# Kernel optimization log

Measured on AMD Instinct MI355X. Metric: run time of the kernel, lower is better.

Reference implementation:

```python
import jax, jax.numpy as jnp
import numpy as np

B = 16384
IN_DIM = 4096
H1, H2 = 128, 64
LATENT = 32
REPS = 3


def setup_inputs() -> dict:
    key = jax.random.key(0)
    ks = jax.random.split(key, 10)
    def lin(k, fan_in, fan_out):
        bound = 1.0 / np.sqrt(fan_in)
        kw, kb = jax.random.split(k)
        W = jax.random.uniform(kw, (fan_in, fan_out), jnp.float32, -bound, bound)
        b = jax.random.uniform(kb, (fan_out,), jnp.float32, -bound, bound)
        return W, b
    x = jax.random.normal(ks[0], (B, IN_DIM), jnp.float32)
    W1, b1 = lin(ks[1], IN_DIM, H1)
    W2, b2 = lin(ks[2], H1, H2)
    W3, b3 = lin(ks[3], H2, LATENT)
    qparams = jax.random.normal(ks[4], (REPS * 2 * LATENT,), jnp.float32)
    Wd, bd = lin(ks[5], LATENT, IN_DIM)
    return {"x": x, "W1": W1, "b1": b1, "W2": W2, "b2": b2,
            "W3": W3, "b3": b3, "qparams": qparams, "Wd": Wd, "bd": bd}


def _forward(x, W1, b1, W2, b2, W3, b3, qparams, Wd, bd):
    # Classical encoder (dropout inactive in eval mode)
    h = jax.nn.relu(x @ W1 + b1)          # [B, H1]
    h = jax.nn.relu(h @ W2 + b2)          # [B, H2]
    z = h @ W3 + b3                       # [B, LATENT]
    # Quantum decoder: circuit is AngleEmbedding (RX) of latent followed by
    # 2*REPS AngleEmbedding (RX) layers of params -- all RX on the same wire
    # commute and add, no entanglers => <Z_i> = cos(total angle on wire i).
    param_offset = qparams.reshape(2 * REPS, LATENT).sum(axis=0)  # [LATENT]
    q = jnp.cos(z + param_offset)         # [B, LATENT]
    # Classical decoder
    return q @ Wd + bd                    # [B, IN_DIM]


def reference(x, W1, b1, W2, b2, W3, b3, qparams, Wd, bd):
    return _forward(x, W1, b1, W2, b2, W3, b3, qparams, Wd, bd)
```

## Files before the change

### kernel.cpp

```cpp
#include <hip/hip_runtime.h>
#include <hip/hip_bf16.h>

#define B_SZ   16384
#define IN_DIM 4096
#define H1D    128
#define H2D    64
#define LAT    32

typedef _Float16 half8 __attribute__((ext_vector_type(8)));
typedef _Float16 half4 __attribute__((ext_vector_type(4)));
typedef float float4v __attribute__((ext_vector_type(4)));

#define WS_W2T  1048576
#define WS_W3T  1064960
#define WS_WDT  1069056
#define WS_B3O  1331200
#define WS_Q    1331328

__global__ __launch_bounds__(256) void prep_kernel(
    const float* __restrict__ W1, const float* __restrict__ W2,
    const float* __restrict__ W3, const float* __restrict__ Wd,
    const float* __restrict__ b3, const float* __restrict__ qp,
    _Float16* __restrict__ W1t, _Float16* __restrict__ W2t,
    _Float16* __restrict__ W3t, _Float16* __restrict__ Wdt,
    float* __restrict__ b3off)
{
    int t = blockIdx.x * 256 + threadIdx.x;
    if (t < IN_DIM * H1D) {
        int k = t >> 7, n = t & 127;
        W1t[n * IN_DIM + k] = (_Float16)W1[t];
    }
    if (t < LAT * IN_DIM) {
        int k = t >> 12, n = t & 4095;
        Wdt[n * LAT + k] = (_Float16)Wd[t];
    }
    if (t < H1D * H2D) {
        int k = t >> 6, n = t & 63;
        W2t[n * H1D + k] = (_Float16)W2[t];
    }
    if (t < H2D * LAT) {
        int k = t >> 5, n = t & 31;
        W3t[n * H2D + k] = (_Float16)W3[t];
    }
    if (t < LAT) {
        float s = b3[t];
        #pragma unroll
        for (int r = 0; r < 6; ++r) s += qp[r * LAT + t];
        b3off[t] = s;
    }
}

__global__ __launch_bounds__(512) void encoder_kernel(
    const float* __restrict__ x,
    const _Float16* __restrict__ W1t, const _Float16* __restrict__ W2t,
    const _Float16* __restrict__ W3t,
    const float* __restrict__ b1, const float* __restrict__ b2,
    const float* __restrict__ b3off, _Float16* __restrict__ qout)
{
    __shared__ alignas(16) char smem[27648];
    _Float16* xt  = (_Float16*)smem;
    _Float16* wt  = (_Float16*)(smem + 9216);
    _Float16* h1s = (_Float16*)smem;
    _Float16* h2s = (_Float16*)(smem + 17408);

    const int tid  = threadIdx.x;
    const int lane = tid & 63;
    const int w    = tid >> 6;
    const int l15  = lane & 15;
    const int quad = lane >> 4;
    const int rb0  = blockIdx.x * 64;

    const int wr = w >> 1;
    const int wc = w & 1;

    float4v acc[4];
    #pragma unroll
    for (int nt = 0; nt < 4; ++nt) {
        float bv = b1[wc * 64 + nt * 16 + l15];
        acc[nt] = (float4v){bv, bv, bv, bv};
    }

    for (int kit = 0; kit < IN_DIM / 64; ++kit) {
        #pragma unroll
        for (int i = 0; i < 2; ++i) {
            int idx = tid + i * 512;
            int r   = idx >> 4;
            int c4  = idx & 15;
            float4v xv = ((const float4v*)(x + (size_t)(rb0 + r) * IN_DIM + kit * 64))[c4];
            half4 p;
            p[0] = (_Float16)xv[0]; p[1] = (_Float16)xv[1];
            p[2] = (_Float16)xv[2]; p[3] = (_Float16)xv[3];
            *(half4*)(xt + r * 72 + c4 * 4) = p;
        }
        #pragma unroll
        for (int i = 0; i < 2; ++i) {
            int idx = tid + i * 512;
            int n   = idx >> 3;
            int c   = idx & 7;
            uint4 v = ((const uint4*)(W1t + (size_t)n * IN_DIM + kit * 64))[c];
            *(uint4*)(wt + n * 72 + c * 8) = v;
        }
        __syncthreads();
        #pragma unroll
        for (int ks = 0; ks < 2; ++ks) {
            half8 a = *(const half8*)(xt + (wr * 16 + l15) * 72 + ks * 32 + quad * 8);
            #pragma unroll
            for (int nt = 0; nt < 4; ++nt) {
                half8 b = *(const half8*)(wt + (wc * 64 + nt * 16 + l15) * 72 + ks * 32 + quad * 8);
                acc[nt] = __builtin_amdgcn_mfma_f32_16x16x32_f16(a, b, acc[nt], 0, 0, 0);
            }
        }
        __syncthreads();
    }

    #pragma unroll
    for (int nt = 0; nt < 4; ++nt) {
        int c = wc * 64 + nt * 16 + l15;
        #pragma unroll
        for (int r = 0; r < 4; ++r) {
            int row = wr * 16 + quad * 4 + r;
            float v = acc[nt][r];
            h1s[row * 136 + c] = (_Float16)(v > 0.f ? v : 0.f);
        }
    }
    __syncthreads();

    const int rb2 = (w & 3) * 16;
    const int wc2 = w >> 2;
    float4v acc2[2];
    #pragma unroll
    for (int nt = 0; nt < 2; ++nt) {
        float bv = b2[wc2 * 32 + nt * 16 + l15];
        acc2[nt] = (float4v){bv, bv, bv, bv};
    }
    #pragma unroll
    for (int ks = 0; ks < 4; ++ks) {
        half8 a = *(const half8*)(h1s + (rb2 + l15) * 136 + ks * 32 + quad * 8);
        #pragma unroll
        for (int nt = 0; nt < 2; ++nt) {
            int n = wc2 * 32 + nt * 16 + l15;
            half8 b = *(const half8*)(W2t + n * H1D + ks * 32 + quad * 8);
            acc2[nt] = __builtin_amdgcn_mfma_f32_16x16x32_f16(a, b, acc2[nt], 0, 0, 0);
        }
    }
    #pragma unroll
    for (int nt = 0; nt < 2; ++nt) {
        int c = wc2 * 32 + nt * 16 + l15;
        #pragma unroll
        for (int r = 0; r < 4; ++r) {
            int row = rb2 + quad * 4 + r;
            float v = acc2[nt][r];
            h2s[row * 72 + c] = (_Float16)(v > 0.f ? v : 0.f);
        }
    }
    __syncthreads();

    const int rb3 = (w & 3) * 16;
    const int wc3 = w >> 2;
    int c3 = wc3 * 16 + l15;
    float bv3 = b3off[c3];
    float4v acc3 = (float4v){bv3, bv3, bv3, bv3};
    #pragma unroll
    for (int ks = 0; ks < 2; ++ks) {
        half8 a = *(const half8*)(h2s + (rb3 + l15) * 72 + ks * 32 + quad * 8);
        half8 b = *(const half8*)(W3t + c3 * H2D + ks * 32 + quad * 8);
        acc3 = __builtin_amdgcn_mfma_f32_16x16x32_f16(a, b, acc3, 0, 0, 0);
    }
    #pragma unroll
    for (int r = 0; r < 4; ++r) {
        int row = rb0 + rb3 + quad * 4 + r;
        qout[(size_t)row * LAT + c3] = (_Float16)cosf(acc3[r]);
    }
}

__global__ __launch_bounds__(256) void decoder_kernel(
    const _Float16* __restrict__ qin, const _Float16* __restrict__ Wdt,
    const float* __restrict__ bd, float* __restrict__ out)
{
    __shared__ alignas(16) _Float16 qs[64 * 40];
    const int tid  = threadIdx.x;
    const int lane = tid & 63;
    const int w    = tid >> 6;
    const int l15  = lane & 15;
    const int quad = lane >> 4;
    const int rowBlk = blockIdx.x & 255;
    const int colBlk = blockIdx.x >> 8;
    const int rb = rowBlk * 64;
    const int cb = colBlk * 256 + w * 64;

    {
        int r = tid >> 2;
        int c = tid & 3;
        uint4 v = *((const uint4*)(qin + (size_t)(rb + r) * LAT) + c);
        *(uint4*)(qs + r * 40 + c * 8) = v;
    }
    __syncthreads();

    half8 a[4];
    #pragma unroll
    for (int mt = 0; mt < 4; ++mt)
        a[mt] = *(const half8*)(qs + (mt * 16 + l15) * 40 + quad * 8);

    #pragma unroll
    for (int nt = 0; nt < 4; ++nt) {
        int c = cb + nt * 16 + l15;
        half8 b = *(const half8*)(Wdt + (size_t)c * LAT + quad * 8);
        float bv = bd[c];
        float4v bias = (float4v){bv, bv, bv, bv};
        #pragma unroll
        for (int mt = 0; mt < 4; ++mt) {
            float4v o = __builtin_amdgcn_mfma_f32_16x16x32_f16(a[mt], b, bias, 0, 0, 0);
            #pragma unroll
            for (int r = 0; r < 4; ++r) {
                out[(size_t)(rb + mt * 16 + quad * 4 + r) * IN_DIM + c] = o[r];
            }
        }
    }
}

extern "C" void kernel_launch(void* const* d_in, const int* in_sizes, int n_in,
                              void* d_out, int out_size, void* d_ws, size_t ws_size,
                              hipStream_t stream)
{
    const float* x  = (const float*)d_in[0];
    const float* W1 = (const float*)d_in[1];
    const float* b1 = (const float*)d_in[2];
    const float* W2 = (const float*)d_in[3];
    const float* b2 = (const float*)d_in[4];
    const float* W3 = (const float*)d_in[5];
    const float* b3 = (const float*)d_in[6];
    const float* qp = (const float*)d_in[7];
    const float* Wd = (const float*)d_in[8];
    const float* bd = (const float*)d_in[9];
    float* out = (float*)d_out;

    char* ws = (char*)d_ws;
    _Float16* W1t = (_Float16*)(ws);
    _Float16* W2t = (_Float16*)(ws + WS_W2T);
    _Float16* W3t = (_Float16*)(ws + WS_W3T);
    _Float16* Wdt = (_Float16*)(ws + WS_WDT);
    float*    b3o = (float*)(ws + WS_B3O);
    _Float16* qbuf= (_Float16*)(ws + WS_Q);

    prep_kernel<<<2048, 256, 0, stream>>>(W1, W2, W3, Wd, b3, qp, W1t, W2t, W3t, Wdt, b3o);
    encoder_kernel<<<256, 512, 0, stream>>>(x, W1t, W2t, W3t, b1, b2, b3o, qbuf);
    decoder_kernel<<<4096, 256, 0, stream>>>(qbuf, Wdt, bd, out);
}
```

Baseline: 585.5 us.

## Use split-K register-direct encoder and LDS-staged coalesced decoder stores

The encoder now uses 32-row blocks with 256 threads, and each wave handles a quarter of the K dimension. Each wave loads x and W1t straight from global memory into MFMA operands without LDS staging or per-iteration barriers. The four partial sums are then reduced through shared memory before the small layers run. The decoder stages each 64x256 output tile in LDS and writes it back as row-contiguous float4 stores, and its block order is changed so consecutive blocks share rows. This trades extra LDS use and lower occupancy for fewer barriers, better parallelism with 512 blocks, and fully coalesced output writes.

```diff
diff --git a/kernel.cpp b/kernel.cpp
--- a/kernel.cpp
+++ b/kernel.cpp
@@ -50,143 +50,153 @@
     }
 }
 
-__global__ __launch_bounds__(512) void encoder_kernel(
+static __device__ __forceinline__ half8 cvt8(float4v v0, float4v v1) {
+    half8 h;
+    h[0] = (_Float16)v0[0]; h[1] = (_Float16)v0[1];
+    h[2] = (_Float16)v0[2]; h[3] = (_Float16)v0[3];
+    h[4] = (_Float16)v1[0]; h[5] = (_Float16)v1[1];
+    h[6] = (_Float16)v1[2]; h[7] = (_Float16)v1[3];
+    return h;
+}
+
+__global__ __launch_bounds__(256, 2) void encoder_kernel(
     const float* __restrict__ x,
     const _Float16* __restrict__ W1t, const _Float16* __restrict__ W2t,
     const _Float16* __restrict__ W3t,
     const float* __restrict__ b1, const float* __restrict__ b2,
     const float* __restrict__ b3off, _Float16* __restrict__ qout)
 {
-    __shared__ alignas(16) char smem[27648];
-    _Float16* xt  = (_Float16*)smem;
-    _Float16* wt  = (_Float16*)(smem + 9216);
-    _Float16* h1s = (_Float16*)smem;
-    _Float16* h2s = (_Float16*)(smem + 17408);
+    __shared__ alignas(16) float part[4 * 32 * 132];
+    __shared__ alignas(16) _Float16 h1s[32 * 136];
+    _Float16* h2s = (_Float16*)part;
 
     const int tid  = threadIdx.x;
     const int lane = tid & 63;
     const int w    = tid >> 6;
     const int l15  = lane & 15;
     const int quad = lane >> 4;
-    const int rb0  = blockIdx.x * 64;
-
-    const int wr = w >> 1;
-    const int wc = w & 1;
-
-    float4v acc[4];
-    #pragma unroll
-    for (int nt = 0; nt < 4; ++nt) {
-        float bv = b1[wc * 64 + nt * 16 + l15];
-        acc[nt] = (float4v){bv, bv, bv, bv};
-    }
-
-    for (int kit = 0; kit < IN_DIM / 64; ++kit) {
-        #pragma unroll
-        for (int i = 0; i < 2; ++i) {
-            int idx = tid + i * 512;
-            int r   = idx >> 4;
-            int c4  = idx & 15;
-            float4v xv = ((const float4v*)(x + (size_t)(rb0 + r) * IN_DIM + kit * 64))[c4];
-            half4 p;
-            p[0] = (_Float16)xv[0]; p[1] = (_Float16)xv[1];
-            p[2] = (_Float16)xv[2]; p[3] = (_Float16)xv[3];
-            *(half4*)(xt + r * 72 + c4 * 4) = p;
-        }
-        #pragma unroll
-        for (int i = 0; i < 2; ++i) {
-            int idx = tid + i * 512;
-            int n   = idx >> 3;
-            int c   = idx & 7;
-            uint4 v = ((const uint4*)(W1t + (size_t)n * IN_DIM + kit * 64))[c];
-            *(uint4*)(wt + n * 72 + c * 8) = v;
+    const int rb0  = blockIdx.x * 32;
+
+    float4v acc[2][8];
+    #pragma unroll
+    for (int mg = 0; mg < 2; ++mg)
+        #pragma unroll
+        for (int ct = 0; ct < 8; ++ct)
+            acc[mg][ct] = (float4v){0.f, 0.f, 0.f, 0.f};
+
+    const float* xp0 = x + (size_t)(rb0 + l15) * IN_DIM + w * 1024 + quad * 8;
+    const float* xp1 = xp0 + 16 * IN_DIM;
+    const _Float16* wp[8];
+    #pragma unroll
+    for (int ct = 0; ct < 8; ++ct)
+        wp[ct] = W1t + (size_t)(ct * 16 + l15) * IN_DIM + w * 1024 + quad * 8;
+
+    #pragma unroll 2
+    for (int kk = 0; kk < 32; ++kk) {
+        const int ko = kk * 32;
+        float4v x00 = *(const float4v*)(xp0 + ko);
+        float4v x01 = *(const float4v*)(xp0 + ko + 4);
+        float4v x10 = *(const float4v*)(xp1 + ko);
+        float4v x11 = *(const float4v*)(xp1 + ko + 4);
+        half8 a0 = cvt8(x00, x01);
+        half8 a1 = cvt8(x10, x11);
+        #pragma unroll
+        for (int ct = 0; ct < 8; ++ct) {
+            half8 b = *(const half8*)(wp[ct] + ko);
+            acc[0][ct] = __builtin_amdgcn_mfma_f32_16x16x32_f16(a0, b, acc[0][ct], 0, 0, 0);
+            acc[1][ct] = __builtin_amdgcn_mfma_f32_16x16x32_f16(a1, b, acc[1][ct], 0, 0, 0);
+        }
+    }
+
+    {
+        float* pw = part + w * (32 * 132);
+        #pragma unroll
+        for (int mg = 0; mg < 2; ++mg)
+            #pragma unroll
+            for (int ct = 0; ct < 8; ++ct)
+                #pragma unroll
+                for (int r = 0; r < 4; ++r)
+                    pw[(mg * 16 + quad * 4 + r) * 132 + ct * 16 + l15] = acc[mg][ct][r];
+    }
+    __syncthreads();
+
+    #pragma unroll
+    for (int i = 0; i < 4; ++i) {
+        int chunk = tid * 4 + i;
+        int row = chunk >> 5;
+        int c4  = chunk & 31;
+        const float* p = part + row * 132 + c4 * 4;
+        float4v s = *(const float4v*)(p)
+                  + *(const float4v*)(p + 32 * 132)
+                  + *(const float4v*)(p + 2 * 32 * 132)
+                  + *(const float4v*)(p + 3 * 32 * 132);
+        float4v bb = *(const float4v*)(b1 + c4 * 4);
+        s = s + bb;
+        half4 h;
+        h[0] = (_Float16)(s[0] > 0.f ? s[0] : 0.f);
+        h[1] = (_Float16)(s[1] > 0.f ? s[1] : 0.f);
+        h[2] = (_Float16)(s[2] > 0.f ? s[2] : 0.f);
+        h[3] = (_Float16)(s[3] > 0.f ? s[3] : 0.f);
+        *(half4*)(h1s + row * 136 + c4 * 4) = h;
+    }
+    __syncthreads();
+
+    {
+        float bv2 = b2[w * 16 + l15];
+        float4v a2[2] = {(float4v){bv2, bv2, bv2, bv2}, (float4v){bv2, bv2, bv2, bv2}};
+        #pragma unroll
+        for (int kk = 0; kk < 4; ++kk) {
+            half8 b = *(const half8*)(W2t + (w * 16 + l15) * H1D + kk * 32 + quad * 8);
+            half8 a0 = *(const half8*)(h1s + l15 * 136 + kk * 32 + quad * 8);
+            half8 a1 = *(const half8*)(h1s + (16 + l15) * 136 + kk * 32 + quad * 8);
+            a2[0] = __builtin_amdgcn_mfma_f32_16x16x32_f16(a0, b, a2[0], 0, 0, 0);
+            a2[1] = __builtin_amdgcn_mfma_f32_16x16x32_f16(a1, b, a2[1], 0, 0, 0);
         }
         __syncthreads();
         #pragma unroll
-        for (int ks = 0; ks < 2; ++ks) {
-            half8 a = *(const half8*)(xt + (wr * 16 + l15) * 72 + ks * 32 + quad * 8);
+        for (int mg = 0; mg < 2; ++mg)
             #pragma unroll
-            for (int nt = 0; nt < 4; ++nt) {
-                half8 b = *(const half8*)(wt + (wc * 64 + nt * 16 + l15) * 72 + ks * 32 + quad * 8);
-                acc[nt] = __builtin_amdgcn_mfma_f32_16x16x32_f16(a, b, acc[nt], 0, 0, 0);
+            for (int r = 0; r < 4; ++r) {
+                float v = a2[mg][r];
+                h2s[(mg * 16 + quad * 4 + r) * 72 + w * 16 + l15] = (_Float16)(v > 0.f ? v : 0.f);
             }
-        }
-        __syncthreads();
-    }
-
-    #pragma unroll
-    for (int nt = 0; nt < 4; ++nt) {
-        int c = wc * 64 + nt * 16 + l15;
+    }
+    __syncthreads();
+
+    {
+        const int mg3 = w >> 1;
+        const int ct3 = w & 1;
+        const int c3  = ct3 * 16 + l15;
+        float bv3 = b3off[c3];
+        float4v a3 = (float4v){bv3, bv3, bv3, bv3};
+        #pragma unroll
+        for (int kk = 0; kk < 2; ++kk) {
+            half8 a = *(const half8*)(h2s + (mg3 * 16 + l15) * 72 + kk * 32 + quad * 8);
+            half8 b = *(const half8*)(W3t + c3 * H2D + kk * 32 + quad * 8);
+            a3 = __builtin_amdgcn_mfma_f32_16x16x32_f16(a, b, a3, 0, 0, 0);
+        }
         #pragma unroll
         for (int r = 0; r < 4; ++r) {
-            int row = wr * 16 + quad * 4 + r;
-            float v = acc[nt][r];
-            h1s[row * 136 + c] = (_Float16)(v > 0.f ? v : 0.f);
-        }
-    }
-    __syncthreads();
-
-    const int rb2 = (w & 3) * 16;
-    const int wc2 = w >> 2;
-    float4v acc2[2];
-    #pragma unroll
-    for (int nt = 0; nt < 2; ++nt) {
-        float bv = b2[wc2 * 32 + nt * 16 + l15];
-        acc2[nt] = (float4v){bv, bv, bv, bv};
-    }
-    #pragma unroll
-    for (int ks = 0; ks < 4; ++ks) {
-        half8 a = *(const half8*)(h1s + (rb2 + l15) * 136 + ks * 32 + quad * 8);
-        #pragma unroll
-        for (int nt = 0; nt < 2; ++nt) {
-            int n = wc2 * 32 + nt * 16 + l15;
-            half8 b = *(const half8*)(W2t + n * H1D + ks * 32 + quad * 8);
-            acc2[nt] = __builtin_amdgcn_mfma_f32_16x16x32_f16(a, b, acc2[nt], 0, 0, 0);
-        }
-    }
-    #pragma unroll
-    for (int nt = 0; nt < 2; ++nt) {
-        int c = wc2 * 32 + nt * 16 + l15;
-        #pragma unroll
-        for (int r = 0; r < 4; ++r) {
-            int row = rb2 + quad * 4 + r;
-            float v = acc2[nt][r];
-            h2s[row * 72 + c] = (_Float16)(v > 0.f ? v : 0.f);
-        }
-    }
-    __syncthreads();
-
-    const int rb3 = (w & 3) * 16;
-    const int wc3 = w >> 2;
-    int c3 = wc3 * 16 + l15;
-    float bv3 = b3off[c3];
-    float4v acc3 = (float4v){bv3, bv3, bv3, bv3};
-    #pragma unroll
-    for (int ks = 0; ks < 2; ++ks) {
-        half8 a = *(const half8*)(h2s + (rb3 + l15) * 72 + ks * 32 + quad * 8);
-        half8 b = *(const half8*)(W3t + c3 * H2D + ks * 32 + quad * 8);
-        acc3 = __builtin_amdgcn_mfma_f32_16x16x32_f16(a, b, acc3, 0, 0, 0);
-    }
-    #pragma unroll
-    for (int r = 0; r < 4; ++r) {
-        int row = rb0 + rb3 + quad * 4 + r;
-        qout[(size_t)row * LAT + c3] = (_Float16)cosf(acc3[r]);
-    }
-}
-
-__global__ __launch_bounds__(256) void decoder_kernel(
+            int row = rb0 + mg3 * 16 + quad * 4 + r;
+            qout[(size_t)row * LAT + c3] = (_Float16)cosf(a3[r]);
+        }
+    }
+}
+
+__global__ __launch_bounds__(256, 2) void decoder_kernel(
     const _Float16* __restrict__ qin, const _Float16* __restrict__ Wdt,
     const float* __restrict__ bd, float* __restrict__ out)
 {
     __shared__ alignas(16) _Float16 qs[64 * 40];
+    __shared__ alignas(16) float ot[64 * 260];
     const int tid  = threadIdx.x;
     const int lane = tid & 63;
     const int w    = tid >> 6;
     const int l15  = lane & 15;
     const int quad = lane >> 4;
-    const int rowBlk = blockIdx.x & 255;
-    const int colBlk = blockIdx.x >> 8;
+    const int rowBlk = blockIdx.x >> 4;
+    const int colBlk = blockIdx.x & 15;
     const int rb = rowBlk * 64;
-    const int cb = colBlk * 256 + w * 64;
 
     {
         int r = tid >> 2;
@@ -203,17 +213,29 @@
 
     #pragma unroll
     for (int nt = 0; nt < 4; ++nt) {
-        int c = cb + nt * 16 + l15;
-        half8 b = *(const half8*)(Wdt + (size_t)c * LAT + quad * 8);
-        float bv = bd[c];
+        int ccol = w * 64 + nt * 16 + l15;
+        int gcol = colBlk * 256 + ccol;
+        half8 b = *(const half8*)(Wdt + (size_t)gcol * LAT + quad * 8);
+        float bv = bd[gcol];
         float4v bias = (float4v){bv, bv, bv, bv};
         #pragma unroll
         for (int mt = 0; mt < 4; ++mt) {
             float4v o = __builtin_amdgcn_mfma_f32_16x16x32_f16(a[mt], b, bias, 0, 0, 0);
             #pragma unroll
-            for (int r = 0; r < 4; ++r) {
-                out[(size_t)(rb + mt * 16 + quad * 4 + r) * IN_DIM + c] = o[r];
-            }
+            for (int r = 0; r < 4; ++r)
+                ot[(mt * 16 + quad * 4 + r) * 260 + ccol] = o[r];
+        }
+    }
+    __syncthreads();
+
+    {
+        const int trow = tid >> 6;
+        const int tcol = (tid & 63) * 4;
+        #pragma unroll
+        for (int r0 = 0; r0 < 64; r0 += 4) {
+            int row = r0 + trow;
+            float4v v = *(const float4v*)(ot + row * 260 + tcol);
+            *(float4v*)(out + (size_t)(rb + row) * IN_DIM + colBlk * 256 + tcol) = v;
         }
     }
 }
@@ -243,6 +265,6 @@
     _Float16* qbuf= (_Float16*)(ws + WS_Q);
 
     prep_kernel<<<2048, 256, 0, stream>>>(W1, W2, W3, Wd, b3, qp, W1t, W2t, W3t, Wdt, b3o);
-    encoder_kernel<<<256, 512, 0, stream>>>(x, W1t, W2t, W3t, b1, b2, b3o, qbuf);
+    encoder_kernel<<<512, 256, 0, stream>>>(x, W1t, W2t, W3t, b1, b2, b3o, qbuf);
     decoder_kernel<<<4096, 256, 0, stream>>>(qbuf, Wdt, bd, out);
 }
```

New measurement: 519.3 us. 11.3% less time.
